# Kernel optimization log

Measured on AMD Instinct MI355X. Metric: run time of the kernel, lower is better.

The kernel has to match this reference:

```python
import jax, jax.numpy as jnp
import numpy as np
from jax.scipy.linalg import expm, solve_triangular

B, N, K, A, V = 2, 256, 16, 16, 32000
ALPHA = 1.0
LAMBDA_BELIEF = 1.0
EPS = 1e-8   # kl_divergence jitter
EPS2 = 1e-6  # pairwise-KL jitter


def _spd(key, b, n, k, scale=0.3):
    a = jax.random.normal(key, (b, n, k, k)) * scale
    return jnp.einsum('bnkl,bnml->bnkm', a, a) + jnp.eye(k)


def setup_inputs() -> dict:
    key = jax.random.key(0)
    ks = jax.random.split(key, 9)
    mu = jax.random.normal(ks[0], (B, N, K))
    Sigma = _spd(ks[1], B, N, K)
    phi = jax.random.normal(ks[2], (B, N, A)) * 0.05
    mu_prior = jax.random.normal(ks[3], (B, N, K))
    Sigma_prior = _spd(ks[4], B, N, K)
    beta = jax.random.uniform(ks[5], (B, N, N)) / N
    W_out = jax.random.normal(ks[6], (V, K)) * 0.02
    R = jax.random.normal(ks[7], (A, K, K))
    generators = (R - jnp.swapaxes(R, -1, -2)) * 0.1  # skew-symmetric Lie generators
    targets = jax.random.randint(ks[8], (B, N), 0, V)
    return {"mu": mu, "Sigma": Sigma, "phi": phi, "mu_prior": mu_prior,
            "Sigma_prior": Sigma_prior, "beta": beta, "W_out": W_out,
            "generators": generators, "targets": targets}


def _bexpm(M):
    # batched matrix exponential over leading dims
    shape = M.shape
    return jax.vmap(expm)(M.reshape(-1, shape[-2], shape[-1])).reshape(shape)


def _potential(mu, Sigma, phi, mu_prior, Sigma_prior, beta, W_out, generators, targets):
    I = jnp.eye(K, dtype=mu.dtype)

    # --- V_self: alpha * sum_n KL(q_n || p_n), explicit-inverse formulation ---
    Sq = Sigma + EPS * I
    Sp = Sigma_prior + EPS * I
    Sp_inv = jnp.linalg.inv(Sp)
    trace_t = jnp.einsum('bnij,bnji->bn', Sp_inv, Sq)
    dmu = mu_prior - mu
    mahal = jnp.einsum('bni,bnij,bnj->bn', dmu, Sp_inv, dmu)
    logdet = jnp.linalg.slogdet(Sp)[1] - jnp.linalg.slogdet(Sq)[1]
    kl_self = 0.5 * (trace_t + mahal - K + logdet)
    V_self = ALPHA * kl_self.sum(-1)

    # --- V_align: pairwise KL under Lie transport Omega_ij = e^{phi_i G} e^{-phi_j G} ---
    phi_mat = jnp.einsum('bna,aij->bnij', phi, generators)          # (B,N,K,K)
    exp_phi = _bexpm(phi_mat)
    exp_neg_phi = _bexpm(-phi_mat)
    Omega = jnp.einsum('bikl,bjlm->bijkm', exp_phi, exp_neg_phi)    # (B,N,N,K,K)
    mu_t = jnp.einsum('bijkl,bjl->bijk', Omega, mu)                 # (B,N,N,K)
    # Omega Sigma_j Omega^T (congruence -> SPD)
    Sigma_t = jnp.einsum('bijkl,bjlm,bijnm->bijkn', Omega, Sigma, Omega)

    Stp = Sigma_t + EPS2 * I
    L_p = jnp.linalg.cholesky(Stp)                                  # (B,N,N,K,K)
    Sigma_i = jnp.broadcast_to((Sigma + EPS2 * I)[:, :, None], (B, N, N, K, K))
    Y = solve_triangular(L_p, Sigma_i, lower=True)
    Z = solve_triangular(jnp.swapaxes(L_p, -1, -2), Y, lower=False)
    trace_term = jnp.diagonal(Z, axis1=-2, axis2=-1).sum(-1)        # (B,N,N)

    delta = mu_t - mu[:, :, None, :]
    v = solve_triangular(L_p, delta[..., None], lower=True)[..., 0]
    mahal_term = (v ** 2).sum(-1)

    logdet_p = 2.0 * jnp.log(jnp.diagonal(L_p, axis1=-2, axis2=-1) + EPS2).sum(-1)
    L_q = jnp.linalg.cholesky(Sigma + EPS2 * I)                     # (B,N,K,K)
    logdet_q = 2.0 * jnp.log(jnp.diagonal(L_q, axis1=-2, axis2=-1) + EPS2).sum(-1)

    kl_all = 0.5 * (trace_term + mahal_term - K + logdet_p - logdet_q[:, :, None])
    kl_all = jnp.maximum(kl_all, 0.0)
    kl_all = kl_all * (1.0 - jnp.eye(N, dtype=mu.dtype))            # zero diagonal
    V_align = LAMBDA_BELIEF * (beta * kl_all).sum((-2, -1))

    # --- V_ce: cross entropy over W_out projection of mu ---
    logits = jnp.einsum('bnk,vk->bnv', mu, W_out)
    logp = jax.nn.log_softmax(logits, axis=-1)
    ce = -jnp.take_along_axis(logp, targets[..., None], axis=-1)[..., 0]
    V_ce = ce.sum(-1)

    return V_self + V_align + V_ce


def reference(mu, Sigma, phi, mu_prior, Sigma_prior, beta, W_out, generators, targets):
    return _potential(mu, Sigma, phi, mu_prior, Sigma_prior, beta, W_out, generators, targets)
```

## Files before the change

kernel.cpp:

```cpp
#include <hip/hip_runtime.h>
#include <math.h>

#define NB 2
#define NN 256
#define KD 16
#define VV 32000
#define EPS_SELF 1e-8f
#define EPS_AL   1e-6f
#define NNODES (NB*NN)

#define CE_ROWS 8
#define CE_CH   32
#define CE_CHUNK (VV/CE_CH)

#define OFF_MT  0
#define OFF_SH  (NNODES*16)
#define OFF_P   (OFF_SH + NNODES*256)
#define OFF_LD  (OFF_P + NNODES*256)
#define OFF_KLS (OFF_LD + NNODES)
#define OFF_CE  (OFF_KLS + NNODES)
#define OFF_AP  (OFF_CE + NNODES)
#define OFF_CEP (OFF_AP + NNODES)
#define WS_FLOATS (OFF_CEP + NNODES*CE_CH)

#define WAVE_SYNC() asm volatile("s_waitcnt lgkmcnt(0)" ::: "memory")

__device__ __forceinline__ void ld4(float* dst, const float4 v) {
  dst[0] = v.x; dst[1] = v.y; dst[2] = v.z; dst[3] = v.w;
}

__device__ __forceinline__ float dot16a(const float* a, const float* b) {
  float acc = 0.f;
  #pragma unroll
  for (int j = 0; j < 16; ++j) acc = fmaf(a[j], b[j], acc);
  return acc;
}

__device__ __forceinline__ void gj16(float aq[4], const int g, const int c, float* ldacc) {
  #pragma unroll
  for (int k = 0; k < 16; ++k) {
    float d    = __shfl(aq[k & 3], ((k >> 2) << 4) | k);
    float rowk = __shfl(aq[k & 3], ((k >> 2) << 4) | c);
    float ck[4];
    #pragma unroll
    for (int q = 0; q < 4; ++q) ck[q] = __shfl(aq[q], (g << 4) | k);
    if (ldacc) *ldacc += logf(d);
    float dinv = 1.f / d;
    #pragma unroll
    for (int q = 0; q < 4; ++q) {
      int r = 4*g + q;
      float vgen = fmaf(-ck[q] * dinv, rowk, aq[q]);
      aq[q] = (r == k) ? ((c == k) ? dinv : aq[q] * dinv)
                       : ((c == k) ? (-ck[q] * dinv) : vgen);
    }
  }
}

template<int QUIRK>
__device__ __forceinline__ float ge16_logdet(float aq[4], const int g, const int c) {
  float ld = 0.f;
  #pragma unroll
  for (int k = 0; k < 16; ++k) {
    float d    = __shfl(aq[k & 3], ((k >> 2) << 4) | k);
    float rowk = __shfl(aq[k & 3], ((k >> 2) << 4) | c);
    float ck[4];
    #pragma unroll
    for (int q = 0; q < 4; ++q) ck[q] = __shfl(aq[q], (g << 4) | k);
    ld += QUIRK ? 2.f * logf(sqrtf(d) + EPS_AL) : logf(d);
    float dinv = 1.f / d;
    #pragma unroll
    for (int q = 0; q < 4; ++q) {
      int r = 4*g + q;
      float upd = fmaf(-ck[q] * dinv, rowk, aq[q]);
      aq[q] = (r > k && c > k) ? upd : aq[q];
    }
  }
  return ld;
}

__global__ __launch_bounds__(256) void prep_kernel(
    const float* __restrict__ mu, const float* __restrict__ Sigma,
    const float* __restrict__ phi, const float* __restrict__ mu_prior,
    const float* __restrict__ Sigma_prior, const float* __restrict__ gen,
    float* __restrict__ ws)
{
  __shared__ __align__(16) float wl[4][980];
  const int tid = threadIdx.x;
  const int w = tid >> 6, l = tid & 63;
  const int g = l >> 4, c = l & 15;
  const int unit = blockIdx.x * 4 + w;
  const int role = unit & 1, node = unit >> 1;
  float* COLp = &wl[w][0];
  float* ROWp = &wl[w][320];
  float* AUXp = &wl[w][640];

  if (role == 0) {
    float phis[16];
    {
      const float4* p4 = (const float4*)(phi + node*16);
      ld4(phis, p4[0]); ld4(phis+4, p4[1]); ld4(phis+8, p4[2]); ld4(phis+12, p4[3]);
    }
    float x[4] = {0.f, 0.f, 0.f, 0.f};
    #pragma unroll
    for (int aa = 0; aa < 16; ++aa) {
      float4 gq = *(const float4*)(gen + aa*256 + c*16 + 4*g);
      x[0] = fmaf(phis[aa], gq.x, x[0]);
      x[1] = fmaf(phis[aa], gq.y, x[1]);
      x[2] = fmaf(phis[aa], gq.z, x[2]);
      x[3] = fmaf(phis[aa], gq.w, x[3]);
    }
    #pragma unroll
    for (int q = 0; q < 4; ++q) x[q] *= -0.125f;

    #pragma unroll
    for (int q = 0; q < 4; ++q) ROWp[(4*g+q)*20 + c] = x[q];
    WAVE_SYNC();
    float Mrow[4][16];
    #pragma unroll
    for (int q = 0; q < 4; ++q)
      #pragma unroll
      for (int j4 = 0; j4 < 4; ++j4)
        ld4(&Mrow[q][4*j4], *(const float4*)&ROWp[(4*g+q)*20 + 4*j4]);

    float t[4];
    #pragma unroll
    for (int q = 0; q < 4; ++q) t[q] = ((4*g+q) == c ? 1.f : 0.f) + x[q]*0.125f;
    for (int k = 7; k >= 1; --k) {
      *(float4*)&COLp[c*20 + 4*g] = make_float4(t[0], t[1], t[2], t[3]);
      WAVE_SYNC();
      float T[16];
      #pragma unroll
      for (int j4 = 0; j4 < 4; ++j4) ld4(&T[4*j4], *(const float4*)&COLp[c*20 + 4*j4]);
      #pragma unroll
      for (int q = 0; q < 4; ++q)
        t[q] = ((4*g+q) == c ? 1.f : 0.f) + dot16a(Mrow[q], T) / (float)k;
    }
    for (int s = 0; s < 3; ++s) {
      *(float4*)&COLp[c*20 + 4*g] = make_float4(t[0], t[1], t[2], t[3]);
      #pragma unroll
      for (int q = 0; q < 4; ++q) ROWp[(4*g+q)*20 + c] = t[q];
      WAVE_SYNC();
      float T[16];
      #pragma unroll
      for (int j4 = 0; j4 < 4; ++j4) ld4(&T[4*j4], *(const float4*)&COLp[c*20 + 4*j4]);
      float nt[4];
      #pragma unroll
      for (int q = 0; q < 4; ++q) {
        float acc = 0.f;
        #pragma unroll
        for (int j4 = 0; j4 < 4; ++j4) {
          float4 rv = *(const float4*)&ROWp[(4*g+q)*20 + 4*j4];
          acc = fmaf(rv.x, T[4*j4+0], acc);
          acc = fmaf(rv.y, T[4*j4+1], acc);
          acc = fmaf(rv.z, T[4*j4+2], acc);
          acc = fmaf(rv.w, T[4*j4+3], acc);
        }
        nt[q] = acc;
      }
      #pragma unroll
      for (int q = 0; q < 4; ++q) t[q] = nt[q];
    }
    *(float4*)&COLp[c*20 + 4*g] = make_float4(t[0], t[1], t[2], t[3]);
    WAVE_SYNC();
    float Ecol[16];
    #pragma unroll
    for (int j4 = 0; j4 < 4; ++j4) ld4(&Ecol[4*j4], *(const float4*)&COLp[c*20 + 4*j4]);

    float w1q[4];
    #pragma unroll
    for (int q = 0; q < 4; ++q) {
      float S[16];
      const float4* s4 = (const float4*)(Sigma + node*256 + (4*g+q)*16);
      ld4(S, s4[0]); ld4(S+4, s4[1]); ld4(S+8, s4[2]); ld4(S+12, s4[3]);
      w1q[q] = dot16a(S, Ecol);
    }
    *(float4*)&AUXp[c*20 + 4*g] = make_float4(w1q[0], w1q[1], w1q[2], w1q[3]);
    WAVE_SYNC();
    float W1c[16];
    #pragma unroll
    for (int j4 = 0; j4 < 4; ++j4) ld4(&W1c[4*j4], *(const float4*)&AUXp[c*20 + 4*j4]);

    float sh[4];
    #pragma unroll
    for (int q = 0; q < 4; ++q) {
      float Er[16];
      #pragma unroll
      for (int j4 = 0; j4 < 4; ++j4) ld4(&Er[4*j4], *(const float4*)&COLp[(4*g+q)*20 + 4*j4]);
      sh[q] = dot16a(Er, W1c) + ((4*g+q) == c ? EPS_AL : 0.f);
    }
    *(float4*)(ws + OFF_SH + node*256 + c*16 + 4*g) = make_float4(sh[0], sh[1], sh[2], sh[3]);

    {
      float muv[16];
      const float4* m4 = (const float4*)(mu + node*16);
      ld4(muv, m4[0]); ld4(muv+4, m4[1]); ld4(muv+8, m4[2]); ld4(muv+12, m4[3]);
      float mt = dot16a(Ecol, muv);
      if (g == 0) ws[OFF_MT + node*16 + c] = mt;
    }
    gj16(sh, g, c, (float*)nullptr);
    *(float4*)(ws + OFF_P + node*256 + c*16 + 4*g) = make_float4(sh[0], sh[1], sh[2], sh[3]);
  } else {
    float sp[4];
    {
      float4 v = *(const float4*)(Sigma_prior + node*256 + c*16 + 4*g);
      sp[0] = v.x + ((4*g+0 == c) ? EPS_SELF : 0.f);
      sp[1] = v.y + ((4*g+1 == c) ? EPS_SELF : 0.f);
      sp[2] = v.z + ((4*g+2 == c) ? EPS_SELF : 0.f);
      sp[3] = v.w + ((4*g+3 == c) ? EPS_SELF : 0.f);
    }
    float ldSp = 0.f;
    gj16(sp, g, c, &ldSp);

    float dmur[4], dmuc;
    {
      float4 a = *(const float4*)(mu_prior + node*16 + 4*g);
      float4 b = *(const float4*)(mu + node*16 + 4*g);
      dmur[0] = a.x - b.x; dmur[1] = a.y - b.y; dmur[2] = a.z - b.z; dmur[3] = a.w - b.w;
      dmuc = mu_prior[node*16 + c] - mu[node*16 + c];
    }
    float val = 0.f;
    {
      float4 v = *(const float4*)(Sigma + node*256 + c*16 + 4*g);
      float s0 = v.x + ((4*g+0 == c) ? EPS_SELF : 0.f);
      float s1 = v.y + ((4*g+1 == c) ? EPS_SELF : 0.f);
      float s2 = v.z + ((4*g+2 == c) ? EPS_SELF : 0.f);
      float s3 = v.w + ((4*g+3 == c) ? EPS_SELF : 0.f);
      val = fmaf(sp[0], s0 + dmur[0]*dmuc, val);
      val = fmaf(sp[1], s1 + dmur[1]*dmuc, val);
      val = fmaf(sp[2], s2 + dmur[2]*dmuc, val);
      val = fmaf(sp[3], s3 + dmur[3]*dmuc, val);
    }
    #pragma unroll
    for (int o = 32; o; o >>= 1) val += __shfl_xor(val, o);

    float sq[4];
    {
      float4 v = *(const float4*)(Sigma + node*256 + c*16 + 4*g);
      sq[0] = v.x + ((4*g+0 == c) ? EPS_SELF : 0.f);
      sq[1] = v.y + ((4*g+1 == c) ? EPS_SELF : 0.f);
      sq[2] = v.z + ((4*g+2 == c) ? EPS_SELF : 0.f);
      sq[3] = v.w + ((4*g+3 == c) ? EPS_SELF : 0.f);
    }
    float ldSq = ge16_logdet<0>(sq, g, c);
    float sg[4];
    {
      float4 v = *(const float4*)(Sigma + node*256 + c*16 + 4*g);
      sg[0] = v.x + ((4*g+0 == c) ? EPS_AL : 0.f);
      sg[1] = v.y + ((4*g+1 == c) ? EPS_AL : 0.f);
      sg[2] = v.z + ((4*g+2 == c) ? EPS_AL : 0.f);
      sg[3] = v.w + ((4*g+3 == c) ? EPS_AL : 0.f);
    }
    float ldq = ge16_logdet<1>(sg, g, c);
    if (l == 0) {
      ws[OFF_KLS + node] = 0.5f * (val - 16.f + ldSp - ldSq);
      ws[OFF_LD + node]  = ldq;
    }
  }
}

#define PSTR 260
__global__ __launch_bounds__(256) void align_kernel(
    const float* __restrict__ beta, const float* __restrict__ wsc, float* __restrict__ ws)
{
  __shared__ __align__(16) float ShI[16*PSTR];
  __shared__ __align__(16) float PJ[16*PSTR];
  __shared__ float mtI[256], mtJ[256], ldI[16], ldJ[16], red[4];
  const int tid = threadIdx.x;
  const int ti = tid & 15, tj = tid >> 4;
  const int bx = blockIdx.x, by = blockIdx.y, bz = blockIdx.z;
  const int nodeI0 = bz*256 + by*16, nodeJ0 = bz*256 + bx*16;

  for (int idx = tid; idx < 16*256; idx += 256) {
    int row = idx >> 8, col = idx & 255;
    ShI[row*PSTR + col] = wsc[OFF_SH + (nodeI0 + row)*256 + col];
    PJ [row*PSTR + col] = wsc[OFF_P  + (nodeJ0 + row)*256 + col];
  }
  mtI[tid] = wsc[OFF_MT + nodeI0*16 + tid];
  mtJ[tid] = wsc[OFF_MT + nodeJ0*16 + tid];
  if (tid < 16) { ldI[tid] = wsc[OFF_LD + nodeI0 + tid]; ldJ[tid] = wsc[OFF_LD + nodeJ0 + tid]; }
  __syncthreads();

  const float4* si4 = (const float4*)&ShI[ti*PSTR];
  const float4* pj4 = (const float4*)&PJ[tj*PSTR];
  float tr = 0.f;
  #pragma unroll 16
  for (int t = 0; t < 64; ++t) {
    float4 xv = si4[t], yv = pj4[t];
    tr = fmaf(xv.x, yv.x, tr);
    tr = fmaf(xv.y, yv.y, tr);
    tr = fmaf(xv.z, yv.z, tr);
    tr = fmaf(xv.w, yv.w, tr);
  }

  const float* pj = &PJ[tj*PSTR];
  float d[16];
  #pragma unroll
  for (int k = 0; k < 16; ++k) d[k] = mtJ[tj*16+k] - mtI[ti*16+k];
  float mah = 0.f;
  #pragma unroll
  for (int k = 0; k < 16; ++k) {
    float acc = 0.f;
    #pragma unroll
    for (int ll = 0; ll < 16; ++ll) acc = fmaf(pj[k*16+ll], d[ll], acc);
    mah = fmaf(d[k], acc, mah);
  }

  float kl = 0.5f * (tr + mah - 16.f + ldJ[tj] - ldI[ti]);
  kl = fmaxf(kl, 0.f);
  int gi = by*16 + ti, gj = bx*16 + tj;
  float contrib = (gi == gj) ? 0.f : kl * beta[bz*65536 + gi*256 + gj];
  #pragma unroll
  for (int o = 32; o; o >>= 1) contrib += __shfl_down(contrib, o);
  __syncthreads();
  if ((tid & 63) == 0) red[tid >> 6] = contrib;
  __syncthreads();
  if (tid == 0) ws[OFF_AP + (bz*16 + by)*16 + bx] = red[0] + red[1] + red[2] + red[3];
}

#define DOT16(q0,q1,q2,q3,A) \
  fmaf(q0.x,A[0],fmaf(q0.y,A[1],fmaf(q0.z,A[2],fmaf(q0.w,A[3], \
  fmaf(q1.x,A[4],fmaf(q1.y,A[5],fmaf(q1.z,A[6],fmaf(q1.w,A[7], \
  fmaf(q2.x,A[8],fmaf(q2.y,A[9],fmaf(q2.z,A[10],fmaf(q2.w,A[11], \
  fmaf(q3.x,A[12],fmaf(q3.y,A[13],fmaf(q3.z,A[14],q3.w*A[15])))))))))))))))

__global__ __launch_bounds__(256) void ce1_kernel(
    const float* __restrict__ mu, const float* __restrict__ W,
    float* __restrict__ ws)
{
  __shared__ float mu_s[CE_ROWS*16];
  __shared__ float sred[CE_ROWS*256];
  const int tid = threadIdx.x;
  const int grp = blockIdx.x;
  const int ch  = blockIdx.y;
  const int row0 = grp * CE_ROWS;

  if (tid < CE_ROWS*16) mu_s[tid] = mu[row0*16 + tid];
  __syncthreads();

  float A[CE_ROWS][16];
  #pragma unroll
  for (int r = 0; r < CE_ROWS; ++r)
    #pragma unroll
    for (int k = 0; k < 16; ++k) A[r][k] = mu_s[r*16+k];

  float acc[CE_ROWS];
  #pragma unroll
  for (int r = 0; r < CE_ROWS; ++r) acc[r] = 0.f;

  const float4* W4 = (const float4*)W;
  const int v0 = ch * CE_CHUNK;
  for (int v = v0 + tid; v < v0 + CE_CHUNK; v += 256) {
    float4 q0 = W4[v*4+0], q1 = W4[v*4+1], q2 = W4[v*4+2], q3 = W4[v*4+3];
    #pragma unroll
    for (int r = 0; r < CE_ROWS; ++r) {
      float lg = DOT16(q0,q1,q2,q3,A[r]);
      acc[r] += __expf(lg);
    }
  }

  #pragma unroll
  for (int r = 0; r < CE_ROWS; ++r) sred[r*256 + tid] = acc[r];
  __syncthreads();
  for (int h = 128; h > 0; h >>= 1) {
    if (tid < h) {
      #pragma unroll
      for (int r = 0; r < CE_ROWS; ++r) sred[r*256+tid] += sred[r*256+tid+h];
    }
    __syncthreads();
  }
  if (tid < CE_ROWS) ws[OFF_CEP + (row0 + tid)*CE_CH + ch] = sred[tid*256];
}

__global__ __launch_bounds__(256) void final_kernel(
    const float* __restrict__ mu, const float* __restrict__ W,
    const int* __restrict__ targets, const float* __restrict__ ws,
    float* __restrict__ out)
{
  __shared__ double red[256];
  const int tid = threadIdx.x;
  const int b = blockIdx.x;
  const int row = b*256 + tid;
  float s = 0.f;
  #pragma unroll
  for (int c2 = 0; c2 < CE_CH; ++c2) s += ws[OFF_CEP + row*CE_CH + c2];
  int t = targets[row];
  float dt = 0.f;
  #pragma unroll
  for (int k = 0; k < 16; ++k) dt = fmaf(mu[row*16+k], W[t*16+k], dt);
  double ce = (double)logf(s) - (double)dt;
  red[tid] = (double)ws[OFF_KLS + row] + (double)ws[OFF_AP + row] + ce;
  __syncthreads();
  for (int h = 128; h > 0; h >>= 1) {
    if (tid < h) red[tid] += red[tid + h];
    __syncthreads();
  }
  if (tid == 0) out[b] = (float)red[0];
}

extern "C" void kernel_launch(void* const* d_in, const int* in_sizes, int n_in,
                              void* d_out, int out_size, void* d_ws, size_t ws_size,
                              hipStream_t stream) {
  const float* mu          = (const float*)d_in[0];
  const float* Sigma       = (const float*)d_in[1];
  const float* phi         = (const float*)d_in[2];
  const float* mu_prior    = (const float*)d_in[3];
  const float* Sigma_prior = (const float*)d_in[4];
  const float* beta        = (const float*)d_in[5];
  const float* W_out       = (const float*)d_in[6];
  const float* gen         = (const float*)d_in[7];
  const int*   targets     = (const int*)d_in[8];
  float* out = (float*)d_out;
  float* ws  = (float*)d_ws;
  if (ws_size < (size_t)WS_FLOATS * sizeof(float)) return;

  prep_kernel<<<256, 256, 0, stream>>>(mu, Sigma, phi, mu_prior, Sigma_prior, gen, ws);
  dim3 ag(16, 16, NB);
  align_kernel<<<ag, 256, 0, stream>>>(beta, ws, ws);
  dim3 cg(NNODES/CE_ROWS, CE_CH);
  ce1_kernel<<<cg, 256, 0, stream>>>(mu, W_out, ws);
  final_kernel<<<NB, 256, 0, stream>>>(mu, W_out, targets, ws, out);
}
```

Baseline: 43.36 us.

## Fuse prep with CE partials and align with final reduction via atomic counter

The per-node prep work and the cross-entropy partial-sum computation are merged into one horizontally fused launch, with CE blocks appended after the prep blocks. The final reduction moves into the align kernel as a last-block-done step driven by an atomic counter. This cuts four launches to two and lets the CE work overlap with prep. The CE block reduction now uses wave shuffles instead of a shared-memory tree, and Sigma is loaded once instead of three times. Risks include the added atomic and a serial tail in the last block, and the counter reset depends on block 0 of the first kernel running before the second kernel starts.

```diff
diff --git a/kernel.cpp b/kernel.cpp
--- a/kernel.cpp
+++ b/kernel.cpp
@@ -18,10 +18,10 @@
 #define OFF_P   (OFF_SH + NNODES*256)
 #define OFF_LD  (OFF_P + NNODES*256)
 #define OFF_KLS (OFF_LD + NNODES)
-#define OFF_CE  (OFF_KLS + NNODES)
-#define OFF_AP  (OFF_CE + NNODES)
+#define OFF_AP  (OFF_KLS + NNODES)
 #define OFF_CEP (OFF_AP + NNODES)
-#define WS_FLOATS (OFF_CEP + NNODES*CE_CH)
+#define OFF_CNT (OFF_CEP + NNODES*CE_CH)
+#define WS_FLOATS (OFF_CNT + 4)
 
 #define WAVE_SYNC() asm volatile("s_waitcnt lgkmcnt(0)" ::: "memory")
 
@@ -78,206 +78,258 @@
   return ld;
 }
 
-__global__ __launch_bounds__(256) void prep_kernel(
+#define DOT16(q0,q1,q2,q3,A) \
+  fmaf(q0.x,A[0],fmaf(q0.y,A[1],fmaf(q0.z,A[2],fmaf(q0.w,A[3], \
+  fmaf(q1.x,A[4],fmaf(q1.y,A[5],fmaf(q1.z,A[6],fmaf(q1.w,A[7], \
+  fmaf(q2.x,A[8],fmaf(q2.y,A[9],fmaf(q2.z,A[10],fmaf(q2.w,A[11], \
+  fmaf(q3.x,A[12],fmaf(q3.y,A[13],fmaf(q3.z,A[14],q3.w*A[15])))))))))))))))
+
+__global__ __launch_bounds__(256) void fusedA_kernel(
     const float* __restrict__ mu, const float* __restrict__ Sigma,
     const float* __restrict__ phi, const float* __restrict__ mu_prior,
     const float* __restrict__ Sigma_prior, const float* __restrict__ gen,
-    float* __restrict__ ws)
+    const float* __restrict__ W, float* __restrict__ ws)
 {
-  __shared__ __align__(16) float wl[4][980];
+  __shared__ __align__(16) float smem[4][980];
   const int tid = threadIdx.x;
-  const int w = tid >> 6, l = tid & 63;
-  const int g = l >> 4, c = l & 15;
-  const int unit = blockIdx.x * 4 + w;
-  const int role = unit & 1, node = unit >> 1;
-  float* COLp = &wl[w][0];
-  float* ROWp = &wl[w][320];
-  float* AUXp = &wl[w][640];
-
-  if (role == 0) {
-    float phis[16];
-    {
-      const float4* p4 = (const float4*)(phi + node*16);
-      ld4(phis, p4[0]); ld4(phis+4, p4[1]); ld4(phis+8, p4[2]); ld4(phis+12, p4[3]);
-    }
-    float x[4] = {0.f, 0.f, 0.f, 0.f};
-    #pragma unroll
-    for (int aa = 0; aa < 16; ++aa) {
-      float4 gq = *(const float4*)(gen + aa*256 + c*16 + 4*g);
-      x[0] = fmaf(phis[aa], gq.x, x[0]);
-      x[1] = fmaf(phis[aa], gq.y, x[1]);
-      x[2] = fmaf(phis[aa], gq.z, x[2]);
-      x[3] = fmaf(phis[aa], gq.w, x[3]);
-    }
-    #pragma unroll
-    for (int q = 0; q < 4; ++q) x[q] *= -0.125f;
-
-    #pragma unroll
-    for (int q = 0; q < 4; ++q) ROWp[(4*g+q)*20 + c] = x[q];
-    WAVE_SYNC();
-    float Mrow[4][16];
-    #pragma unroll
-    for (int q = 0; q < 4; ++q)
-      #pragma unroll
-      for (int j4 = 0; j4 < 4; ++j4)
-        ld4(&Mrow[q][4*j4], *(const float4*)&ROWp[(4*g+q)*20 + 4*j4]);
-
-    float t[4];
-    #pragma unroll
-    for (int q = 0; q < 4; ++q) t[q] = ((4*g+q) == c ? 1.f : 0.f) + x[q]*0.125f;
-    for (int k = 7; k >= 1; --k) {
+  const int bid = blockIdx.x;
+
+  if (bid < 256) {
+    if (bid == 0 && tid == 0) *(unsigned*)(ws + OFF_CNT) = 0u;
+    const int w = tid >> 6, l = tid & 63;
+    const int g = l >> 4, c = l & 15;
+    const int unit = bid * 4 + w;
+    const int role = unit & 1, node = unit >> 1;
+    float* COLp = &smem[w][0];
+    float* ROWp = &smem[w][320];
+    float* AUXp = &smem[w][640];
+
+    if (role == 0) {
+      float phis[16];
+      {
+        const float4* p4 = (const float4*)(phi + node*16);
+        ld4(phis, p4[0]); ld4(phis+4, p4[1]); ld4(phis+8, p4[2]); ld4(phis+12, p4[3]);
+      }
+      float x[4] = {0.f, 0.f, 0.f, 0.f};
+      #pragma unroll
+      for (int aa = 0; aa < 16; ++aa) {
+        float4 gq = *(const float4*)(gen + aa*256 + c*16 + 4*g);
+        x[0] = fmaf(phis[aa], gq.x, x[0]);
+        x[1] = fmaf(phis[aa], gq.y, x[1]);
+        x[2] = fmaf(phis[aa], gq.z, x[2]);
+        x[3] = fmaf(phis[aa], gq.w, x[3]);
+      }
+      #pragma unroll
+      for (int q = 0; q < 4; ++q) x[q] *= -0.125f;
+
+      #pragma unroll
+      for (int q = 0; q < 4; ++q) ROWp[(4*g+q)*20 + c] = x[q];
+      WAVE_SYNC();
+      float Mrow[4][16];
+      #pragma unroll
+      for (int q = 0; q < 4; ++q)
+        #pragma unroll
+        for (int j4 = 0; j4 < 4; ++j4)
+          ld4(&Mrow[q][4*j4], *(const float4*)&ROWp[(4*g+q)*20 + 4*j4]);
+
+      float t[4];
+      #pragma unroll
+      for (int q = 0; q < 4; ++q) t[q] = ((4*g+q) == c ? 1.f : 0.f) + x[q]*0.125f;
+      for (int k = 7; k >= 1; --k) {
+        *(float4*)&COLp[c*20 + 4*g] = make_float4(t[0], t[1], t[2], t[3]);
+        WAVE_SYNC();
+        float T[16];
+        #pragma unroll
+        for (int j4 = 0; j4 < 4; ++j4) ld4(&T[4*j4], *(const float4*)&COLp[c*20 + 4*j4]);
+        #pragma unroll
+        for (int q = 0; q < 4; ++q)
+          t[q] = ((4*g+q) == c ? 1.f : 0.f) + dot16a(Mrow[q], T) / (float)k;
+      }
+      for (int s = 0; s < 3; ++s) {
+        *(float4*)&COLp[c*20 + 4*g] = make_float4(t[0], t[1], t[2], t[3]);
+        #pragma unroll
+        for (int q = 0; q < 4; ++q) ROWp[(4*g+q)*20 + c] = t[q];
+        WAVE_SYNC();
+        float T[16];
+        #pragma unroll
+        for (int j4 = 0; j4 < 4; ++j4) ld4(&T[4*j4], *(const float4*)&COLp[c*20 + 4*j4]);
+        float nt[4];
+        #pragma unroll
+        for (int q = 0; q < 4; ++q) {
+          float acc = 0.f;
+          #pragma unroll
+          for (int j4 = 0; j4 < 4; ++j4) {
+            float4 rv = *(const float4*)&ROWp[(4*g+q)*20 + 4*j4];
+            acc = fmaf(rv.x, T[4*j4+0], acc);
+            acc = fmaf(rv.y, T[4*j4+1], acc);
+            acc = fmaf(rv.z, T[4*j4+2], acc);
+            acc = fmaf(rv.w, T[4*j4+3], acc);
+          }
+          nt[q] = acc;
+        }
+        #pragma unroll
+        for (int q = 0; q < 4; ++q) t[q] = nt[q];
+      }
       *(float4*)&COLp[c*20 + 4*g] = make_float4(t[0], t[1], t[2], t[3]);
       WAVE_SYNC();
-      float T[16];
-      #pragma unroll
-      for (int j4 = 0; j4 < 4; ++j4) ld4(&T[4*j4], *(const float4*)&COLp[c*20 + 4*j4]);
-      #pragma unroll
-      for (int q = 0; q < 4; ++q)
-        t[q] = ((4*g+q) == c ? 1.f : 0.f) + dot16a(Mrow[q], T) / (float)k;
-    }
-    for (int s = 0; s < 3; ++s) {
-      *(float4*)&COLp[c*20 + 4*g] = make_float4(t[0], t[1], t[2], t[3]);
-      #pragma unroll
-      for (int q = 0; q < 4; ++q) ROWp[(4*g+q)*20 + c] = t[q];
+      float Ecol[16];
+      #pragma unroll
+      for (int j4 = 0; j4 < 4; ++j4) ld4(&Ecol[4*j4], *(const float4*)&COLp[c*20 + 4*j4]);
+
+      float w1q[4];
+      #pragma unroll
+      for (int q = 0; q < 4; ++q) {
+        float S[16];
+        const float4* s4 = (const float4*)(Sigma + node*256 + (4*g+q)*16);
+        ld4(S, s4[0]); ld4(S+4, s4[1]); ld4(S+8, s4[2]); ld4(S+12, s4[3]);
+        w1q[q] = dot16a(S, Ecol);
+      }
+      *(float4*)&AUXp[c*20 + 4*g] = make_float4(w1q[0], w1q[1], w1q[2], w1q[3]);
       WAVE_SYNC();
-      float T[16];
-      #pragma unroll
-      for (int j4 = 0; j4 < 4; ++j4) ld4(&T[4*j4], *(const float4*)&COLp[c*20 + 4*j4]);
-      float nt[4];
+      float W1c[16];
+      #pragma unroll
+      for (int j4 = 0; j4 < 4; ++j4) ld4(&W1c[4*j4], *(const float4*)&AUXp[c*20 + 4*j4]);
+
+      float sh[4];
       #pragma unroll
       for (int q = 0; q < 4; ++q) {
-        float acc = 0.f;
-        #pragma unroll
-        for (int j4 = 0; j4 < 4; ++j4) {
-          float4 rv = *(const float4*)&ROWp[(4*g+q)*20 + 4*j4];
-          acc = fmaf(rv.x, T[4*j4+0], acc);
-          acc = fmaf(rv.y, T[4*j4+1], acc);
-          acc = fmaf(rv.z, T[4*j4+2], acc);
-          acc = fmaf(rv.w, T[4*j4+3], acc);
-        }
-        nt[q] = acc;
-      }
-      #pragma unroll
-      for (int q = 0; q < 4; ++q) t[q] = nt[q];
-    }
-    *(float4*)&COLp[c*20 + 4*g] = make_float4(t[0], t[1], t[2], t[3]);
-    WAVE_SYNC();
-    float Ecol[16];
-    #pragma unroll
-    for (int j4 = 0; j4 < 4; ++j4) ld4(&Ecol[4*j4], *(const float4*)&COLp[c*20 + 4*j4]);
-
-    float w1q[4];
-    #pragma unroll
-    for (int q = 0; q < 4; ++q) {
-      float S[16];
-      const float4* s4 = (const float4*)(Sigma + node*256 + (4*g+q)*16);
-      ld4(S, s4[0]); ld4(S+4, s4[1]); ld4(S+8, s4[2]); ld4(S+12, s4[3]);
-      w1q[q] = dot16a(S, Ecol);
-    }
-    *(float4*)&AUXp[c*20 + 4*g] = make_float4(w1q[0], w1q[1], w1q[2], w1q[3]);
-    WAVE_SYNC();
-    float W1c[16];
-    #pragma unroll
-    for (int j4 = 0; j4 < 4; ++j4) ld4(&W1c[4*j4], *(const float4*)&AUXp[c*20 + 4*j4]);
-
-    float sh[4];
-    #pragma unroll
-    for (int q = 0; q < 4; ++q) {
-      float Er[16];
-      #pragma unroll
-      for (int j4 = 0; j4 < 4; ++j4) ld4(&Er[4*j4], *(const float4*)&COLp[(4*g+q)*20 + 4*j4]);
-      sh[q] = dot16a(Er, W1c) + ((4*g+q) == c ? EPS_AL : 0.f);
-    }
-    *(float4*)(ws + OFF_SH + node*256 + c*16 + 4*g) = make_float4(sh[0], sh[1], sh[2], sh[3]);
-
-    {
-      float muv[16];
-      const float4* m4 = (const float4*)(mu + node*16);
-      ld4(muv, m4[0]); ld4(muv+4, m4[1]); ld4(muv+8, m4[2]); ld4(muv+12, m4[3]);
-      float mt = dot16a(Ecol, muv);
-      if (g == 0) ws[OFF_MT + node*16 + c] = mt;
-    }
-    gj16(sh, g, c, (float*)nullptr);
-    *(float4*)(ws + OFF_P + node*256 + c*16 + 4*g) = make_float4(sh[0], sh[1], sh[2], sh[3]);
+        float Er[16];
+        #pragma unroll
+        for (int j4 = 0; j4 < 4; ++j4) ld4(&Er[4*j4], *(const float4*)&COLp[(4*g+q)*20 + 4*j4]);
+        sh[q] = dot16a(Er, W1c) + ((4*g+q) == c ? EPS_AL : 0.f);
+      }
+      *(float4*)(ws + OFF_SH + node*256 + c*16 + 4*g) = make_float4(sh[0], sh[1], sh[2], sh[3]);
+
+      {
+        float muv[16];
+        const float4* m4 = (const float4*)(mu + node*16);
+        ld4(muv, m4[0]); ld4(muv+4, m4[1]); ld4(muv+8, m4[2]); ld4(muv+12, m4[3]);
+        float mt = dot16a(Ecol, muv);
+        if (g == 0) ws[OFF_MT + node*16 + c] = mt;
+      }
+      gj16(sh, g, c, (float*)nullptr);
+      *(float4*)(ws + OFF_P + node*256 + c*16 + 4*g) = make_float4(sh[0], sh[1], sh[2], sh[3]);
+    } else {
+      float sp[4];
+      {
+        float4 v = *(const float4*)(Sigma_prior + node*256 + c*16 + 4*g);
+        sp[0] = v.x + ((4*g+0 == c) ? EPS_SELF : 0.f);
+        sp[1] = v.y + ((4*g+1 == c) ? EPS_SELF : 0.f);
+        sp[2] = v.z + ((4*g+2 == c) ? EPS_SELF : 0.f);
+        sp[3] = v.w + ((4*g+3 == c) ? EPS_SELF : 0.f);
+      }
+      float ldSp = 0.f;
+      gj16(sp, g, c, &ldSp);
+
+      float dmur[4], dmuc;
+      {
+        float4 a = *(const float4*)(mu_prior + node*16 + 4*g);
+        float4 b = *(const float4*)(mu + node*16 + 4*g);
+        dmur[0] = a.x - b.x; dmur[1] = a.y - b.y; dmur[2] = a.z - b.z; dmur[3] = a.w - b.w;
+        dmuc = mu_prior[node*16 + c] - mu[node*16 + c];
+      }
+      float4 sv = *(const float4*)(Sigma + node*256 + c*16 + 4*g);
+      float val = 0.f;
+      {
+        float s0 = sv.x + ((4*g+0 == c) ? EPS_SELF : 0.f);
+        float s1 = sv.y + ((4*g+1 == c) ? EPS_SELF : 0.f);
+        float s2 = sv.z + ((4*g+2 == c) ? EPS_SELF : 0.f);
+        float s3 = sv.w + ((4*g+3 == c) ? EPS_SELF : 0.f);
+        val = fmaf(sp[0], s0 + dmur[0]*dmuc, val);
+        val = fmaf(sp[1], s1 + dmur[1]*dmuc, val);
+        val = fmaf(sp[2], s2 + dmur[2]*dmuc, val);
+        val = fmaf(sp[3], s3 + dmur[3]*dmuc, val);
+      }
+      #pragma unroll
+      for (int o = 32; o; o >>= 1) val += __shfl_xor(val, o);
+
+      float sq[4];
+      sq[0] = sv.x + ((4*g+0 == c) ? EPS_SELF : 0.f);
+      sq[1] = sv.y + ((4*g+1 == c) ? EPS_SELF : 0.f);
+      sq[2] = sv.z + ((4*g+2 == c) ? EPS_SELF : 0.f);
+      sq[3] = sv.w + ((4*g+3 == c) ? EPS_SELF : 0.f);
+      float ldSq = ge16_logdet<0>(sq, g, c);
+      float sg[4];
+      sg[0] = sv.x + ((4*g+0 == c) ? EPS_AL : 0.f);
+      sg[1] = sv.y + ((4*g+1 == c) ? EPS_AL : 0.f);
+      sg[2] = sv.z + ((4*g+2 == c) ? EPS_AL : 0.f);
+      sg[3] = sv.w + ((4*g+3 == c) ? EPS_AL : 0.f);
+      float ldq = ge16_logdet<1>(sg, g, c);
+      if (l == 0) {
+        ws[OFF_KLS + node] = 0.5f * (val - 16.f + ldSp - ldSq);
+        ws[OFF_LD + node]  = ldq;
+      }
+    }
   } else {
-    float sp[4];
-    {
-      float4 v = *(const float4*)(Sigma_prior + node*256 + c*16 + 4*g);
-      sp[0] = v.x + ((4*g+0 == c) ? EPS_SELF : 0.f);
-      sp[1] = v.y + ((4*g+1 == c) ? EPS_SELF : 0.f);
-      sp[2] = v.z + ((4*g+2 == c) ? EPS_SELF : 0.f);
-      sp[3] = v.w + ((4*g+3 == c) ? EPS_SELF : 0.f);
-    }
-    float ldSp = 0.f;
-    gj16(sp, g, c, &ldSp);
-
-    float dmur[4], dmuc;
-    {
-      float4 a = *(const float4*)(mu_prior + node*16 + 4*g);
-      float4 b = *(const float4*)(mu + node*16 + 4*g);
-      dmur[0] = a.x - b.x; dmur[1] = a.y - b.y; dmur[2] = a.z - b.z; dmur[3] = a.w - b.w;
-      dmuc = mu_prior[node*16 + c] - mu[node*16 + c];
-    }
-    float val = 0.f;
-    {
-      float4 v = *(const float4*)(Sigma + node*256 + c*16 + 4*g);
-      float s0 = v.x + ((4*g+0 == c) ? EPS_SELF : 0.f);
-      float s1 = v.y + ((4*g+1 == c) ? EPS_SELF : 0.f);
-      float s2 = v.z + ((4*g+2 == c) ? EPS_SELF : 0.f);
-      float s3 = v.w + ((4*g+3 == c) ? EPS_SELF : 0.f);
-      val = fmaf(sp[0], s0 + dmur[0]*dmuc, val);
-      val = fmaf(sp[1], s1 + dmur[1]*dmuc, val);
-      val = fmaf(sp[2], s2 + dmur[2]*dmuc, val);
-      val = fmaf(sp[3], s3 + dmur[3]*dmuc, val);
-    }
-    #pragma unroll
-    for (int o = 32; o; o >>= 1) val += __shfl_xor(val, o);
-
-    float sq[4];
-    {
-      float4 v = *(const float4*)(Sigma + node*256 + c*16 + 4*g);
-      sq[0] = v.x + ((4*g+0 == c) ? EPS_SELF : 0.f);
-      sq[1] = v.y + ((4*g+1 == c) ? EPS_SELF : 0.f);
-      sq[2] = v.z + ((4*g+2 == c) ? EPS_SELF : 0.f);
-      sq[3] = v.w + ((4*g+3 == c) ? EPS_SELF : 0.f);
-    }
-    float ldSq = ge16_logdet<0>(sq, g, c);
-    float sg[4];
-    {
-      float4 v = *(const float4*)(Sigma + node*256 + c*16 + 4*g);
-      sg[0] = v.x + ((4*g+0 == c) ? EPS_AL : 0.f);
-      sg[1] = v.y + ((4*g+1 == c) ? EPS_AL : 0.f);
-      sg[2] = v.z + ((4*g+2 == c) ? EPS_AL : 0.f);
-      sg[3] = v.w + ((4*g+3 == c) ? EPS_AL : 0.f);
-    }
-    float ldq = ge16_logdet<1>(sg, g, c);
+    const int idx = bid - 256;
+    const int grp = idx & 63;
+    const int ch  = idx >> 6;
+    const int row0 = grp * CE_ROWS;
+    float* mu_s = &smem[0][0];
+    float* wred = &smem[0][128];
+
+    if (tid < CE_ROWS*16) mu_s[tid] = mu[row0*16 + tid];
+    __syncthreads();
+
+    float A[CE_ROWS][16];
+    #pragma unroll
+    for (int r = 0; r < CE_ROWS; ++r)
+      #pragma unroll
+      for (int k = 0; k < 16; ++k) A[r][k] = mu_s[r*16+k];
+
+    float acc[CE_ROWS];
+    #pragma unroll
+    for (int r = 0; r < CE_ROWS; ++r) acc[r] = 0.f;
+
+    const float4* W4 = (const float4*)W;
+    const int v0 = ch * CE_CHUNK;
+    for (int v = v0 + tid; v < v0 + CE_CHUNK; v += 256) {
+      float4 q0 = W4[v*4+0], q1 = W4[v*4+1], q2 = W4[v*4+2], q3 = W4[v*4+3];
+      #pragma unroll
+      for (int r = 0; r < CE_ROWS; ++r) {
+        float lg = DOT16(q0,q1,q2,q3,A[r]);
+        acc[r] += __expf(lg);
+      }
+    }
+    #pragma unroll
+    for (int r = 0; r < CE_ROWS; ++r)
+      #pragma unroll
+      for (int o = 32; o; o >>= 1) acc[r] += __shfl_xor(acc[r], o);
+    const int w = tid >> 6, l = tid & 63;
     if (l == 0) {
-      ws[OFF_KLS + node] = 0.5f * (val - 16.f + ldSp - ldSq);
-      ws[OFF_LD + node]  = ldq;
-    }
+      #pragma unroll
+      for (int r = 0; r < CE_ROWS; ++r) wred[w*CE_ROWS + r] = acc[r];
+    }
+    __syncthreads();
+    if (tid < CE_ROWS)
+      ws[OFF_CEP + (row0 + tid)*CE_CH + ch] =
+          wred[tid] + wred[CE_ROWS + tid] + wred[2*CE_ROWS + tid] + wred[3*CE_ROWS + tid];
   }
 }
 
 #define PSTR 260
-__global__ __launch_bounds__(256) void align_kernel(
-    const float* __restrict__ beta, const float* __restrict__ wsc, float* __restrict__ ws)
+__global__ __launch_bounds__(256) void alignB_kernel(
+    const float* __restrict__ beta, const float* __restrict__ mu,
+    const float* __restrict__ W, const int* __restrict__ targets,
+    float* __restrict__ ws, float* __restrict__ out)
 {
   __shared__ __align__(16) float ShI[16*PSTR];
   __shared__ __align__(16) float PJ[16*PSTR];
   __shared__ float mtI[256], mtJ[256], ldI[16], ldJ[16], red[4];
+  __shared__ int lastflag;
   const int tid = threadIdx.x;
   const int ti = tid & 15, tj = tid >> 4;
-  const int bx = blockIdx.x, by = blockIdx.y, bz = blockIdx.z;
+  const int bx = blockIdx.x & 15, by = (blockIdx.x >> 4) & 15, bz = blockIdx.x >> 8;
   const int nodeI0 = bz*256 + by*16, nodeJ0 = bz*256 + bx*16;
 
   for (int idx = tid; idx < 16*256; idx += 256) {
     int row = idx >> 8, col = idx & 255;
-    ShI[row*PSTR + col] = wsc[OFF_SH + (nodeI0 + row)*256 + col];
-    PJ [row*PSTR + col] = wsc[OFF_P  + (nodeJ0 + row)*256 + col];
-  }
-  mtI[tid] = wsc[OFF_MT + nodeI0*16 + tid];
-  mtJ[tid] = wsc[OFF_MT + nodeJ0*16 + tid];
-  if (tid < 16) { ldI[tid] = wsc[OFF_LD + nodeI0 + tid]; ldJ[tid] = wsc[OFF_LD + nodeJ0 + tid]; }
+    ShI[row*PSTR + col] = ws[OFF_SH + (nodeI0 + row)*256 + col];
+    PJ [row*PSTR + col] = ws[OFF_P  + (nodeJ0 + row)*256 + col];
+  }
+  mtI[tid] = ws[OFF_MT + nodeI0*16 + tid];
+  mtJ[tid] = ws[OFF_MT + nodeJ0*16 + tid];
+  if (tid < 16) { ldI[tid] = ws[OFF_LD + nodeI0 + tid]; ldJ[tid] = ws[OFF_LD + nodeJ0 + tid]; }
   __syncthreads();
 
   const float4* si4 = (const float4*)&ShI[ti*PSTR];
@@ -314,87 +366,47 @@
   __syncthreads();
   if ((tid & 63) == 0) red[tid >> 6] = contrib;
   __syncthreads();
-  if (tid == 0) ws[OFF_AP + (bz*16 + by)*16 + bx] = red[0] + red[1] + red[2] + red[3];
-}
-
-#define DOT16(q0,q1,q2,q3,A) \
-  fmaf(q0.x,A[0],fmaf(q0.y,A[1],fmaf(q0.z,A[2],fmaf(q0.w,A[3], \
-  fmaf(q1.x,A[4],fmaf(q1.y,A[5],fmaf(q1.z,A[6],fmaf(q1.w,A[7], \
-  fmaf(q2.x,A[8],fmaf(q2.y,A[9],fmaf(q2.z,A[10],fmaf(q2.w,A[11], \
-  fmaf(q3.x,A[12],fmaf(q3.y,A[13],fmaf(q3.z,A[14],q3.w*A[15])))))))))))))))
-
-__global__ __launch_bounds__(256) void ce1_kernel(
-    const float* __restrict__ mu, const float* __restrict__ W,
-    float* __restrict__ ws)
-{
-  __shared__ float mu_s[CE_ROWS*16];
-  __shared__ float sred[CE_ROWS*256];
-  const int tid = threadIdx.x;
-  const int grp = blockIdx.x;
-  const int ch  = blockIdx.y;
-  const int row0 = grp * CE_ROWS;
-
-  if (tid < CE_ROWS*16) mu_s[tid] = mu[row0*16 + tid];
+  if (tid == 0) {
+    ws[OFF_AP + (bz*16 + by)*16 + bx] = red[0] + red[1] + red[2] + red[3];
+    unsigned old = __hip_atomic_fetch_add((unsigned*)(ws + OFF_CNT), 1u,
+                                          __ATOMIC_ACQ_REL, __HIP_MEMORY_SCOPE_AGENT);
+    lastflag = (old == 511u);
+  }
   __syncthreads();
 
-  float A[CE_ROWS][16];
-  #pragma unroll
-  for (int r = 0; r < CE_ROWS; ++r)
-    #pragma unroll
-    for (int k = 0; k < 16; ++k) A[r][k] = mu_s[r*16+k];
-
-  float acc[CE_ROWS];
-  #pragma unroll
-  for (int r = 0; r < CE_ROWS; ++r) acc[r] = 0.f;
-
-  const float4* W4 = (const float4*)W;
-  const int v0 = ch * CE_CHUNK;
-  for (int v = v0 + tid; v < v0 + CE_CHUNK; v += 256) {
-    float4 q0 = W4[v*4+0], q1 = W4[v*4+1], q2 = W4[v*4+2], q3 = W4[v*4+3];
-    #pragma unroll
-    for (int r = 0; r < CE_ROWS; ++r) {
-      float lg = DOT16(q0,q1,q2,q3,A[r]);
-      acc[r] += __expf(lg);
-    }
-  }
-
-  #pragma unroll
-  for (int r = 0; r < CE_ROWS; ++r) sred[r*256 + tid] = acc[r];
-  __syncthreads();
-  for (int h = 128; h > 0; h >>= 1) {
-    if (tid < h) {
-      #pragma unroll
-      for (int r = 0; r < CE_ROWS; ++r) sred[r*256+tid] += sred[r*256+tid+h];
-    }
-    __syncthreads();
-  }
-  if (tid < CE_ROWS) ws[OFF_CEP + (row0 + tid)*CE_CH + ch] = sred[tid*256];
-}
-
-__global__ __launch_bounds__(256) void final_kernel(
-    const float* __restrict__ mu, const float* __restrict__ W,
-    const int* __restrict__ targets, const float* __restrict__ ws,
-    float* __restrict__ out)
-{
-  __shared__ double red[256];
-  const int tid = threadIdx.x;
-  const int b = blockIdx.x;
-  const int row = b*256 + tid;
-  float s = 0.f;
-  #pragma unroll
-  for (int c2 = 0; c2 < CE_CH; ++c2) s += ws[OFF_CEP + row*CE_CH + c2];
-  int t = targets[row];
-  float dt = 0.f;
-  #pragma unroll
-  for (int k = 0; k < 16; ++k) dt = fmaf(mu[row*16+k], W[t*16+k], dt);
-  double ce = (double)logf(s) - (double)dt;
-  red[tid] = (double)ws[OFF_KLS + row] + (double)ws[OFF_AP + row] + ce;
-  __syncthreads();
-  for (int h = 128; h > 0; h >>= 1) {
-    if (tid < h) red[tid] += red[tid + h];
-    __syncthreads();
-  }
-  if (tid == 0) out[b] = (float)red[0];
+  if (lastflag) {
+    double* dred = (double*)ShI;
+    double v[2];
+    #pragma unroll
+    for (int b = 0; b < 2; ++b) {
+      int row = b*256 + tid;
+      float s = 0.f;
+      #pragma unroll
+      for (int c2 = 0; c2 < CE_CH; ++c2) s += ws[OFF_CEP + row*CE_CH + c2];
+      int t = targets[row];
+      float dt = 0.f;
+      const float4* wt4 = (const float4*)(W + t*16);
+      const float4* mr4 = (const float4*)(mu + row*16);
+      #pragma unroll
+      for (int j4 = 0; j4 < 4; ++j4) {
+        float4 a = mr4[j4], bb = wt4[j4];
+        dt = fmaf(a.x, bb.x, dt); dt = fmaf(a.y, bb.y, dt);
+        dt = fmaf(a.z, bb.z, dt); dt = fmaf(a.w, bb.w, dt);
+      }
+      double ce = (double)logf(s) - (double)dt;
+      v[b] = (double)ws[OFF_KLS + row] + (double)ws[OFF_AP + row] + ce;
+    }
+    for (int b = 0; b < 2; ++b) {
+      dred[tid] = v[b];
+      __syncthreads();
+      for (int h = 128; h > 0; h >>= 1) {
+        if (tid < h) dred[tid] += dred[tid + h];
+        __syncthreads();
+      }
+      if (tid == 0) out[b] = (float)dred[0];
+      __syncthreads();
+    }
+  }
 }
 
 extern "C" void kernel_launch(void* const* d_in, const int* in_sizes, int n_in,
@@ -413,10 +425,7 @@
   float* ws  = (float*)d_ws;
   if (ws_size < (size_t)WS_FLOATS * sizeof(float)) return;
 
-  prep_kernel<<<256, 256, 0, stream>>>(mu, Sigma, phi, mu_prior, Sigma_prior, gen, ws);
-  dim3 ag(16, 16, NB);
-  align_kernel<<<ag, 256, 0, stream>>>(beta, ws, ws);
-  dim3 cg(NNODES/CE_ROWS, CE_CH);
-  ce1_kernel<<<cg, 256, 0, stream>>>(mu, W_out, ws);
-  final_kernel<<<NB, 256, 0, stream>>>(mu, W_out, targets, ws, out);
-}
+  fusedA_kernel<<<256 + (NNODES/CE_ROWS)*CE_CH, 256, 0, stream>>>(
+      mu, Sigma, phi, mu_prior, Sigma_prior, gen, W_out, ws);
+  alignB_kernel<<<NB*16*16, 256, 0, stream>>>(beta, mu, W_out, targets, ws, out);
+}
```

New measurement: 44.32 us. 1.02x slower.
